# Performance work log

Measured on AMD Instinct MI355X. Metric: run time of the kernel, lower is better.

The kernel has to match this reference:

```python
import jax, jax.numpy as jnp
import numpy as np

N_JOINTS = 50
N_BONES = 50  # mask slicing [:, :, :50] / [:, :, :150] in the source requires exactly 50 bones
# Original repo's getSkeletalModelStructure() is not provided; use deterministic
# bone pairs (i, (i+1) % 50) over the 50 joints. Same gather+norm+direction math.
BONE_A = np.arange(N_JOINTS)
BONE_B = (BONE_A + 1) % N_JOINTS


def _length_direct(x):
    # x: [B, T, 150] -> joints [B, T, 50, 3]
    B, T, _ = x.shape
    joints = x.reshape(B, T, N_JOINTS, 3)
    diff = joints[:, :, BONE_A, :] - joints[:, :, BONE_B, :]  # [B, T, 50, 3]
    length = jnp.linalg.norm(diff, axis=-1)                   # [B, T, 50]
    tiny = jnp.finfo(x.dtype).tiny
    direct = diff / (length[..., None] + tiny)                # [B, T, 50, 3]
    return length, direct.reshape(B, T, N_BONES * 3)          # [B, T, 150]


def setup_inputs() -> dict:
    key = jax.random.key(0)
    k1, k2 = jax.random.split(key)
    shape = (128, 1024, 150)
    return {
        "preds": jax.random.normal(k1, shape, dtype=jnp.float32),
        "targets": jax.random.normal(k2, shape, dtype=jnp.float32),
    }


def reference(preds, targets):
    target_pad = 0.0
    loss_scale = 0.1
    mask = (targets != target_pad).astype(preds.dtype)  # [B, T, 150]
    p = preds * mask
    t = targets * mask
    # lengths are computed in the original but unused in the final loss;
    # only the direction terms enter the bone loss.
    _, p_dir = _length_direct(p)
    _, t_dir = _length_direct(t)
    p_dir = p_dir * mask[:, :, :150]
    t_dir = t_dir * mask[:, :, :150]
    loss = jnp.mean(jnp.abs(p - t)) + 0.1 * jnp.mean((p_dir - t_dir) ** 2)
    return loss * loss_scale
```

## Files before the change

kernel.cpp:

```cpp
#include <hip/hip_runtime.h>

constexpr int   FRAMES   = 128 * 1024;
constexpr int   NB       = 50;
constexpr int   FRAME_F  = 150;
constexpr float TINY     = 1.17549435e-38f;
constexpr float SCALE    = 0.1f / (float)(FRAMES * FRAME_F);

constexpr int FPB   = 32;
constexpr int FLTS  = FPB * FRAME_F;
constexpr int VECS  = FLTS / 4;
constexpr int NBLK  = FRAMES / FPB;
constexpr int TASKS = FPB * NB;

__global__ __launch_bounds__(256) void bone_loss_main(
    const float* __restrict__ preds,
    const float* __restrict__ targets,
    float* __restrict__ partials)
{
    __shared__ float4 sp4[VECS];
    __shared__ float4 st4[VECS];
    float* sp = (float*)sp4;
    float* st = (float*)st4;

    const long base = (long)blockIdx.x * FLTS;
    const float4* gp = (const float4*)(preds + base);
    const float4* gt = (const float4*)(targets + base);
    #pragma unroll
    for (int i = threadIdx.x; i < VECS; i += 256) {
        sp4[i] = gp[i];
        st4[i] = gt[i];
    }
    __syncthreads();

    float acc = 0.0f;
    for (int t = threadIdx.x; t < TASKS; t += 256) {
        const int f  = t / NB;
        const int b  = t - f * NB;
        const int jb = (b == NB - 1) ? 0 : b + 1;
        const int bi = f * FRAME_F + b * 3;
        const int bj = f * FRAME_F + jb * 3;

        const float p0 = sp[bi],   p1 = sp[bi+1], p2 = sp[bi+2];
        const float q0 = sp[bj],   q1 = sp[bj+1], q2 = sp[bj+2];
        const float t0 = st[bi],   t1 = st[bi+1], t2 = st[bi+2];
        const float u0 = st[bj],   u1 = st[bj+1], u2 = st[bj+2];

        const float m0 = (t0 != 0.0f) ? 1.0f : 0.0f;
        const float m1 = (t1 != 0.0f) ? 1.0f : 0.0f;
        const float m2 = (t2 != 0.0f) ? 1.0f : 0.0f;
        const float n0 = (u0 != 0.0f) ? 1.0f : 0.0f;
        const float n1 = (u1 != 0.0f) ? 1.0f : 0.0f;
        const float n2 = (u2 != 0.0f) ? 1.0f : 0.0f;

        const float pm0 = p0 * m0, pm1 = p1 * m1, pm2 = p2 * m2;
        const float qm0 = q0 * n0, qm1 = q1 * n1, qm2 = q2 * n2;

        const float ab = fabsf(pm0 - t0) + fabsf(pm1 - t1) + fabsf(pm2 - t2);

        const float pd0 = pm0 - qm0, pd1 = pm1 - qm1, pd2 = pm2 - qm2;
        const float td0 = t0  - u0,  td1 = t1  - u1,  td2 = t2  - u2;

        const float plen = sqrtf(pd0*pd0 + pd1*pd1 + pd2*pd2);
        const float tlen = sqrtf(td0*td0 + td1*td1 + td2*td2);
        const float pri  = 1.0f / (plen + TINY);
        const float tri  = 1.0f / (tlen + TINY);

        const float d0 = pd0 * pri * m0 - td0 * tri * m0;
        const float d1 = pd1 * pri * m1 - td1 * tri * m1;
        const float d2 = pd2 * pri * m2 - td2 * tri * m2;

        acc += ab + 0.1f * (d0*d0 + d1*d1 + d2*d2);
    }

    #pragma unroll
    for (int off = 32; off > 0; off >>= 1)
        acc += __shfl_down(acc, off, 64);

    __shared__ float ws[4];
    const int lane = threadIdx.x & 63;
    const int wid  = threadIdx.x >> 6;
    if (lane == 0) ws[wid] = acc;
    __syncthreads();
    if (threadIdx.x == 0)
        partials[blockIdx.x] = ws[0] + ws[1] + ws[2] + ws[3];
}

__global__ __launch_bounds__(256) void bone_loss_finish(
    const float* __restrict__ partials,
    float* __restrict__ out)
{
    float v = 0.0f;
    for (int i = threadIdx.x; i < NBLK; i += 256)
        v += partials[i];

    #pragma unroll
    for (int off = 32; off > 0; off >>= 1)
        v += __shfl_down(v, off, 64);

    __shared__ float ws[4];
    const int lane = threadIdx.x & 63;
    const int wid  = threadIdx.x >> 6;
    if (lane == 0) ws[wid] = v;
    __syncthreads();
    if (threadIdx.x == 0)
        out[0] = (ws[0] + ws[1] + ws[2] + ws[3]) * SCALE;
}

extern "C" void kernel_launch(void* const* d_in, const int* in_sizes, int n_in,
                              void* d_out, int out_size, void* d_ws, size_t ws_size,
                              hipStream_t stream) {
    const float* preds   = (const float*)d_in[0];
    const float* targets = (const float*)d_in[1];
    float* out      = (float*)d_out;
    float* partials = (float*)d_ws;

    bone_loss_main<<<NBLK, 256, 0, stream>>>(preds, targets, partials);
    bone_loss_finish<<<1, 256, 0, stream>>>(partials, out);
}
```

Before: 180.2 us.

## Map one wave per frame group, load joints directly and shuffle neighbors

Replaces the LDS staging of 32-frame tiles with a wave-per-16-frames scheme. Each lane loads its own joint's three coordinates straight from global memory, prefetches the next frame's values, and obtains the neighbouring joint through cross-lane shuffles instead of shared memory reads. The sqrt plus divide with a tiny epsilon becomes a hardware rsq guarded by a zero check. The aim is to remove LDS traffic, barriers and integer div/mod, at the cost of non-vectorized strided 3-float global loads, 14 idle lanes per wave, and approximate rsq precision.

```diff
diff --git a/kernel.cpp b/kernel.cpp
--- a/kernel.cpp
+++ b/kernel.cpp
@@ -3,73 +3,75 @@
 constexpr int   FRAMES   = 128 * 1024;
 constexpr int   NB       = 50;
 constexpr int   FRAME_F  = 150;
-constexpr float TINY     = 1.17549435e-38f;
 constexpr float SCALE    = 0.1f / (float)(FRAMES * FRAME_F);
 
-constexpr int FPB   = 32;
-constexpr int FLTS  = FPB * FRAME_F;
-constexpr int VECS  = FLTS / 4;
-constexpr int NBLK  = FRAMES / FPB;
-constexpr int TASKS = FPB * NB;
+constexpr int FPW    = 16;
+constexpr int NWAVES = FRAMES / FPW;
+constexpr int BLOCK  = 256;
+constexpr int NBLK   = NWAVES * 64 / BLOCK;
 
 __global__ __launch_bounds__(256) void bone_loss_main(
     const float* __restrict__ preds,
     const float* __restrict__ targets,
     float* __restrict__ partials)
 {
-    __shared__ float4 sp4[VECS];
-    __shared__ float4 st4[VECS];
-    float* sp = (float*)sp4;
-    float* st = (float*)st4;
+    const int gid   = blockIdx.x * BLOCK + threadIdx.x;
+    const int wave  = gid >> 6;
+    const int lane  = threadIdx.x & 63;
+    const bool act  = lane < NB;
+    const int  jcl  = act ? lane : (NB - 1);
+    const int  sidx = (lane >= NB - 1) ? lane - (NB - 1) : lane + 1;
 
-    const long base = (long)blockIdx.x * FLTS;
-    const float4* gp = (const float4*)(preds + base);
-    const float4* gt = (const float4*)(targets + base);
-    #pragma unroll
-    for (int i = threadIdx.x; i < VECS; i += 256) {
-        sp4[i] = gp[i];
-        st4[i] = gt[i];
-    }
-    __syncthreads();
+    const long fbase = (long)wave * FPW;
+    const float* pp = preds   + fbase * FRAME_F + jcl * 3;
+    const float* tp = targets + fbase * FRAME_F + jcl * 3;
 
     float acc = 0.0f;
-    for (int t = threadIdx.x; t < TASKS; t += 256) {
-        const int f  = t / NB;
-        const int b  = t - f * NB;
-        const int jb = (b == NB - 1) ? 0 : b + 1;
-        const int bi = f * FRAME_F + b * 3;
-        const int bj = f * FRAME_F + jb * 3;
 
-        const float p0 = sp[bi],   p1 = sp[bi+1], p2 = sp[bi+2];
-        const float q0 = sp[bj],   q1 = sp[bj+1], q2 = sp[bj+2];
-        const float t0 = st[bi],   t1 = st[bi+1], t2 = st[bi+2];
-        const float u0 = st[bj],   u1 = st[bj+1], u2 = st[bj+2];
+    float p0 = pp[0], p1 = pp[1], p2 = pp[2];
+    float t0 = tp[0], t1 = tp[1], t2 = tp[2];
+
+    #pragma unroll
+    for (int i = 0; i < FPW; ++i) {
+        float np0 = 0.f, np1 = 0.f, np2 = 0.f, nt0 = 0.f, nt1 = 0.f, nt2 = 0.f;
+        if (i + 1 < FPW) {
+            const float* npp = pp + (i + 1) * FRAME_F;
+            const float* ntp = tp + (i + 1) * FRAME_F;
+            np0 = npp[0]; np1 = npp[1]; np2 = npp[2];
+            nt0 = ntp[0]; nt1 = ntp[1]; nt2 = ntp[2];
+        }
 
         const float m0 = (t0 != 0.0f) ? 1.0f : 0.0f;
         const float m1 = (t1 != 0.0f) ? 1.0f : 0.0f;
         const float m2 = (t2 != 0.0f) ? 1.0f : 0.0f;
-        const float n0 = (u0 != 0.0f) ? 1.0f : 0.0f;
-        const float n1 = (u1 != 0.0f) ? 1.0f : 0.0f;
-        const float n2 = (u2 != 0.0f) ? 1.0f : 0.0f;
-
         const float pm0 = p0 * m0, pm1 = p1 * m1, pm2 = p2 * m2;
-        const float qm0 = q0 * n0, qm1 = q1 * n1, qm2 = q2 * n2;
 
         const float ab = fabsf(pm0 - t0) + fabsf(pm1 - t1) + fabsf(pm2 - t2);
+
+        const float qm0 = __shfl(pm0, sidx, 64);
+        const float qm1 = __shfl(pm1, sidx, 64);
+        const float qm2 = __shfl(pm2, sidx, 64);
+        const float u0  = __shfl(t0,  sidx, 64);
+        const float u1  = __shfl(t1,  sidx, 64);
+        const float u2  = __shfl(t2,  sidx, 64);
 
         const float pd0 = pm0 - qm0, pd1 = pm1 - qm1, pd2 = pm2 - qm2;
         const float td0 = t0  - u0,  td1 = t1  - u1,  td2 = t2  - u2;
 
-        const float plen = sqrtf(pd0*pd0 + pd1*pd1 + pd2*pd2);
-        const float tlen = sqrtf(td0*td0 + td1*td1 + td2*td2);
-        const float pri  = 1.0f / (plen + TINY);
-        const float tri  = 1.0f / (tlen + TINY);
+        const float pl2 = pd0*pd0 + pd1*pd1 + pd2*pd2;
+        const float tl2 = td0*td0 + td1*td1 + td2*td2;
+        const float pri = (pl2 > 0.0f) ? __builtin_amdgcn_rsqf(pl2) : 0.0f;
+        const float tri = (tl2 > 0.0f) ? __builtin_amdgcn_rsqf(tl2) : 0.0f;
 
-        const float d0 = pd0 * pri * m0 - td0 * tri * m0;
-        const float d1 = pd1 * pri * m1 - td1 * tri * m1;
-        const float d2 = pd2 * pri * m2 - td2 * tri * m2;
+        const float d0 = pd0 * pri - td0 * tri;
+        const float d1 = pd1 * pri - td1 * tri;
+        const float d2 = pd2 * pri - td2 * tri;
+        const float sq = m0*d0*d0 + m1*d1*d1 + m2*d2*d2;
 
-        acc += ab + 0.1f * (d0*d0 + d1*d1 + d2*d2);
+        acc += act ? (ab + 0.1f * sq) : 0.0f;
+
+        p0 = np0; p1 = np1; p2 = np2;
+        t0 = nt0; t1 = nt1; t2 = nt2;
     }
 
     #pragma unroll
@@ -77,9 +79,8 @@
         acc += __shfl_down(acc, off, 64);
 
     __shared__ float ws[4];
-    const int lane = threadIdx.x & 63;
-    const int wid  = threadIdx.x >> 6;
-    if (lane == 0) ws[wid] = acc;
+    const int wid = threadIdx.x >> 6;
+    if ((threadIdx.x & 63) == 0) ws[wid] = acc;
     __syncthreads();
     if (threadIdx.x == 0)
         partials[blockIdx.x] = ws[0] + ws[1] + ws[2] + ws[3];
@@ -98,9 +99,8 @@
         v += __shfl_down(v, off, 64);
 
     __shared__ float ws[4];
-    const int lane = threadIdx.x & 63;
-    const int wid  = threadIdx.x >> 6;
-    if (lane == 0) ws[wid] = v;
+    const int wid = threadIdx.x >> 6;
+    if ((threadIdx.x & 63) == 0) ws[wid] = v;
     __syncthreads();
     if (threadIdx.x == 0)
         out[0] = (ws[0] + ws[1] + ws[2] + ws[3]) * SCALE;
@@ -114,6 +114,6 @@
     float* out      = (float*)d_out;
     float* partials = (float*)d_ws;
 
-    bone_loss_main<<<NBLK, 256, 0, stream>>>(preds, targets, partials);
+    bone_loss_main<<<NBLK, BLOCK, 0, stream>>>(preds, targets, partials);
     bone_loss_finish<<<1, 256, 0, stream>>>(partials, out);
 }
```

Result: faster. 175.6 us (-2.5%).
